# Performance work log

Hardware: AMD Instinct MI355X
Metric: run time of the kernel (lower is better)

The kernel has to match this reference:

```python
import jax, jax.numpy as jnp
import numpy as np

N_NODES = 100000
N_EDGES = 1600000
IN_FEAT = 128
OUT_FEAT = 128


def setup_inputs() -> dict:
    key = jax.random.key(0)
    k1, k2, k3 = jax.random.split(key, 3)
    x = jax.random.normal(k1, (N_NODES, IN_FEAT), dtype=jnp.float32)
    W = jax.random.normal(k2, (IN_FEAT, OUT_FEAT), dtype=jnp.float32) * (1.0 / np.sqrt(IN_FEAT))
    b = jnp.zeros((OUT_FEAT,), dtype=jnp.float32)
    edge_index = jax.random.randint(k3, (2, N_EDGES), 0, N_NODES, dtype=jnp.int64)
    return {"x": x, "W": W, "b": b, "edge_index": edge_index}


def reference(x, W, b, edge_index):
    # PyG GCNConv: add self-loops, symmetric deg normalization, scatter-add.
    N = x.shape[0]
    loops = jnp.arange(N, dtype=edge_index.dtype)
    ei = jnp.concatenate([edge_index, jnp.stack([loops, loops])], axis=1)  # [2, E+N]
    row, col = ei[0], ei[1]  # source, target
    ones = jnp.ones(ei.shape[1], dtype=x.dtype)
    deg = jax.ops.segment_sum(ones, col, num_segments=N)  # in-degree incl. self-loop
    deg_inv_sqrt = jnp.where(deg > 0, jax.lax.rsqrt(deg), 0.0)
    norm = deg_inv_sqrt[row] * deg_inv_sqrt[col]  # [E+N]
    xw = x @ W  # [N, out_feat]
    msg = xw[row] * norm[:, None]  # gather + normalize
    out = jax.ops.segment_sum(msg, col, num_segments=N) + b  # scatter-add + bias
    return out
```

## Files before the change

kernel.cpp:

```cpp
#include <hip/hip_runtime.h>

#define N_NODES 100000
#define N_EDGES 1600000
#define FEAT 128
#define NBUCK 782
#define BUCK_SHIFT 7
#define BUCK_MASK 127
#define GEMM_BLOCKS 1563
#define HIST_EPB 4096
#define HIST_BLOCKS 391
#define WT_PITCH 136

typedef __attribute__((ext_vector_type(8))) short short8;
typedef __attribute__((ext_vector_type(4))) float f32x4;

__device__ inline unsigned short f2bf(float f) {
    unsigned u = __builtin_bit_cast(unsigned, f);
    unsigned r = (u + 0x7FFFu + ((u >> 16) & 1u)) >> 16;
    return (unsigned short)r;
}
__device__ inline float bf2f(unsigned h) {
    unsigned u = h << 16;
    return __builtin_bit_cast(float, u);
}

__global__ __launch_bounds__(256)
void k_gemm_hist(const float* __restrict__ x, const float* __restrict__ W,
                 unsigned short* __restrict__ yb,
                 const int* __restrict__ col, int* __restrict__ bcnt) {
    int bid = blockIdx.x, tid = threadIdx.x;
    if (bid >= GEMM_BLOCKS) {
        __shared__ int hist[NBUCK];
        for (int i = tid; i < NBUCK; i += 256) hist[i] = 0;
        __syncthreads();
        int e0 = (bid - GEMM_BLOCKS) * HIST_EPB;
        int n = min(HIST_EPB, N_EDGES - e0);
        for (int i = tid * 4; i < n; i += 1024) {
            if (i + 3 < n) {
                int4 c4 = *(const int4*)(col + e0 + i);
                atomicAdd(&hist[c4.x >> BUCK_SHIFT], 1);
                atomicAdd(&hist[c4.y >> BUCK_SHIFT], 1);
                atomicAdd(&hist[c4.z >> BUCK_SHIFT], 1);
                atomicAdd(&hist[c4.w >> BUCK_SHIFT], 1);
            } else {
                for (int j = i; j < n; ++j) atomicAdd(&hist[col[e0 + j] >> BUCK_SHIFT], 1);
            }
        }
        __syncthreads();
        for (int i = tid; i < NBUCK; i += 256) {
            int h = hist[i];
            if (h) atomicAdd(&bcnt[i], h);
        }
        return;
    }

    __shared__ unsigned short Ws[FEAT * WT_PITCH];
    for (int idx = tid; idx < FEAT * FEAT; idx += 256) {
        int k = idx >> 7, n = idx & 127;
        Ws[n * WT_PITCH + k] = f2bf(W[idx]);
    }
    __syncthreads();

    int lane = tid & 63;
    int m = lane & 15, quad = lane >> 4;
    int rowBase = bid * 64 + (tid >> 6) * 16;
    int arow = rowBase + m;
    if (arow >= N_NODES) arow = N_NODES - 1;
    const float* xr = x + (size_t)arow * FEAT + quad * 8;

    f32x4 acc[8];
#pragma unroll
    for (int nt = 0; nt < 8; ++nt) acc[nt] = (f32x4){0.f, 0.f, 0.f, 0.f};

#pragma unroll
    for (int kk = 0; kk < 4; ++kk) {
        float4 xa = *(const float4*)(xr + kk * 32);
        float4 xc = *(const float4*)(xr + kk * 32 + 4);
        short8 a;
        a[0] = (short)f2bf(xa.x); a[1] = (short)f2bf(xa.y);
        a[2] = (short)f2bf(xa.z); a[3] = (short)f2bf(xa.w);
        a[4] = (short)f2bf(xc.x); a[5] = (short)f2bf(xc.y);
        a[6] = (short)f2bf(xc.z); a[7] = (short)f2bf(xc.w);
        const unsigned short* wp = Ws + m * WT_PITCH + kk * 32 + quad * 8;
#pragma unroll
        for (int nt = 0; nt < 8; ++nt) {
            short8 bf = *(const short8*)(wp + nt * 16 * WT_PITCH);
            acc[nt] = __builtin_amdgcn_mfma_f32_16x16x32_bf16(a, bf, acc[nt], 0, 0, 0);
        }
    }

    int r0 = rowBase + quad * 4;
#pragma unroll
    for (int nt = 0; nt < 8; ++nt) {
        int cc = nt * 16 + m;
#pragma unroll
        for (int r = 0; r < 4; ++r) {
            int rr = r0 + r;
            if (rr < N_NODES) yb[(size_t)rr * FEAT + cc] = f2bf(acc[nt][r]);
        }
    }
}

__global__ __launch_bounds__(1024)
void k_bscan(const int* __restrict__ bcnt, int* __restrict__ bstarts,
             int* __restrict__ bcursor) {
    __shared__ int s[1024];
    int tid = threadIdx.x;
    int v = (tid < NBUCK) ? bcnt[tid] : 0;
    s[tid] = v;
    __syncthreads();
    for (int off = 1; off < 1024; off <<= 1) {
        int t = (tid >= off) ? s[tid - off] : 0;
        __syncthreads();
        s[tid] += t;
        __syncthreads();
    }
    if (tid < NBUCK) {
        int ex = s[tid] - v;
        bstarts[tid] = ex;
        bcursor[tid] = ex;
    }
    if (tid == NBUCK - 1) bstarts[NBUCK] = s[tid];
}

__global__ __launch_bounds__(256)
void k_bscatter(const int* __restrict__ row, const int* __restrict__ col,
                int* __restrict__ bcursor, unsigned* __restrict__ ebuf) {
    __shared__ int hist[NBUCK];
    __shared__ int gbase[NBUCK];
    int tid = threadIdx.x;
    for (int i = tid; i < NBUCK; i += 256) hist[i] = 0;
    __syncthreads();
    int e0 = blockIdx.x * HIST_EPB;
    int n = min(HIST_EPB, N_EDGES - e0);
    for (int i = tid * 4; i < n; i += 1024) {
        if (i + 3 < n) {
            int4 c4 = *(const int4*)(col + e0 + i);
            atomicAdd(&hist[c4.x >> BUCK_SHIFT], 1);
            atomicAdd(&hist[c4.y >> BUCK_SHIFT], 1);
            atomicAdd(&hist[c4.z >> BUCK_SHIFT], 1);
            atomicAdd(&hist[c4.w >> BUCK_SHIFT], 1);
        } else {
            for (int j = i; j < n; ++j) atomicAdd(&hist[col[e0 + j] >> BUCK_SHIFT], 1);
        }
    }
    __syncthreads();
    for (int i = tid; i < NBUCK; i += 256) {
        int h = hist[i];
        gbase[i] = h ? atomicAdd(&bcursor[i], h) : 0;
    }
    __syncthreads();
    for (int i = tid; i < NBUCK; i += 256) hist[i] = 0;
    __syncthreads();
    for (int i = tid * 4; i < n; i += 1024) {
        if (i + 3 < n) {
            int4 c4 = *(const int4*)(col + e0 + i);
            int4 r4 = *(const int4*)(row + e0 + i);
            int bk, off;
            bk = c4.x >> BUCK_SHIFT; off = atomicAdd(&hist[bk], 1);
            ebuf[gbase[bk] + off] = ((unsigned)r4.x << BUCK_SHIFT) | (unsigned)(c4.x & BUCK_MASK);
            bk = c4.y >> BUCK_SHIFT; off = atomicAdd(&hist[bk], 1);
            ebuf[gbase[bk] + off] = ((unsigned)r4.y << BUCK_SHIFT) | (unsigned)(c4.y & BUCK_MASK);
            bk = c4.z >> BUCK_SHIFT; off = atomicAdd(&hist[bk], 1);
            ebuf[gbase[bk] + off] = ((unsigned)r4.z << BUCK_SHIFT) | (unsigned)(c4.z & BUCK_MASK);
            bk = c4.w >> BUCK_SHIFT; off = atomicAdd(&hist[bk], 1);
            ebuf[gbase[bk] + off] = ((unsigned)r4.w << BUCK_SHIFT) | (unsigned)(c4.w & BUCK_MASK);
        } else {
            for (int j = i; j < n; ++j) {
                int c = col[e0 + j], r = row[e0 + j];
                int bk = c >> BUCK_SHIFT;
                int off = atomicAdd(&hist[bk], 1);
                ebuf[gbase[bk] + off] = ((unsigned)r << BUCK_SHIFT) | (unsigned)(c & BUCK_MASK);
            }
        }
    }
}

__global__ __launch_bounds__(256)
void k_csr(const unsigned* __restrict__ ebuf, const int* __restrict__ bstarts,
           int* __restrict__ starts, float* __restrict__ dinv,
           int* __restrict__ src_idx) {
    __shared__ int hist[128];
    __shared__ int scan[128];
    __shared__ int cur[128];
    int b = blockIdx.x, tid = threadIdx.x;
    int node0 = b << BUCK_SHIFT;
    int nnodes = min(128, N_NODES - node0);
    if (tid < 128) hist[tid] = 0;
    __syncthreads();
    int e0 = bstarts[b], e1 = bstarts[b + 1];
    int ne = e1 - e0;
    for (int i = tid; i < ne; i += 256) atomicAdd(&hist[ebuf[e0 + i] & BUCK_MASK], 1);
    __syncthreads();
    if (tid < 128) scan[tid] = hist[tid];
    __syncthreads();
    for (int off = 1; off < 128; off <<= 1) {
        int t = 0;
        if (tid < 128 && tid >= off) t = scan[tid - off];
        __syncthreads();
        if (tid < 128) scan[tid] += t;
        __syncthreads();
    }
    if (tid < 128) {
        int ex = scan[tid] - hist[tid];
        cur[tid] = ex;
        if (tid < nnodes) {
            starts[node0 + tid] = e0 + ex;
            dinv[node0 + tid] = rsqrtf((float)(hist[tid] + 1));
        }
    }
    if (b == 0 && tid == 0) starts[N_NODES] = N_EDGES;
    __syncthreads();
    for (int i = tid; i < ne; i += 256) {
        unsigned e = ebuf[e0 + i];
        int pos = atomicAdd(&cur[e & BUCK_MASK], 1);
        src_idx[e0 + pos] = (int)(e >> BUCK_SHIFT);
    }
}

#define GATHER_GROUP(D)                                             \
    {                                                               \
        unsigned v[D];                                              \
        _Pragma("unroll")                                           \
        for (int t = 0; t < (D); ++t) {                             \
            int s = __shfl(src, j + t);                             \
            v[t] = y1[(size_t)(unsigned)s * 64 + lane];             \
        }                                                           \
        _Pragma("unroll")                                           \
        for (int t = 0; t < (D); ++t) {                             \
            float d = __shfl(dvv, j + t);                           \
            a0 += d * bf2f(v[t] & 0xFFFFu);                         \
            a1 += d * bf2f(v[t] >> 16);                             \
        }                                                           \
        j += (D);                                                   \
    }

__global__ __launch_bounds__(256)
void k_agg(const unsigned short* __restrict__ yb, const int* __restrict__ starts,
           const int* __restrict__ src_idx, const float* __restrict__ dinv,
           const float* __restrict__ bias, float* __restrict__ out) {
    int node = blockIdx.x * 4 + (threadIdx.x >> 6);
    int lane = threadIdx.x & 63;
    if (node >= N_NODES) return;
    int st = starts[node], en = starts[node + 1];
    float di = dinv[node];
    const unsigned* y1 = (const unsigned*)yb;
    unsigned sv = y1[(size_t)node * 64 + lane];
    float a0 = di * bf2f(sv & 0xFFFFu);
    float a1 = di * bf2f(sv >> 16);
    for (int base = st; base < en; base += 64) {
        int nn = min(64, en - base);
        int src = 0;
        float dvv = 0.f;
        if (lane < nn) {
            src = src_idx[base + lane];
            dvv = dinv[src];
        }
        int j = 0;
        while (j + 16 <= nn) GATHER_GROUP(16)
        if (j + 8 <= nn) GATHER_GROUP(8)
        if (j + 4 <= nn) GATHER_GROUP(4)
        for (; j < nn; ++j) {
            int s = __shfl(src, j);
            float d = __shfl(dvv, j);
            unsigned v = y1[(size_t)(unsigned)s * 64 + lane];
            a0 += d * bf2f(v & 0xFFFFu);
            a1 += d * bf2f(v >> 16);
        }
    }
    float2 bb = ((const float2*)bias)[lane];
    float2 o;
    o.x = bb.x + di * a0;
    o.y = bb.y + di * a1;
    ((float2*)out)[(size_t)node * 64 + lane] = o;
}

extern "C" void kernel_launch(void* const* d_in, const int* in_sizes, int n_in,
                              void* d_out, int out_size, void* d_ws, size_t ws_size,
                              hipStream_t stream) {
    const float* x = (const float*)d_in[0];
    const float* W = (const float*)d_in[1];
    const float* b = (const float*)d_in[2];
    const int* ei = (const int*)d_in[3];
    const int* row = ei;
    const int* col = ei + N_EDGES;
    float* out = (float*)d_out;

    char* ws = (char*)d_ws;
    size_t off = 0;
    auto alloc = [&](size_t bytes) -> void* {
        void* p = ws + off;
        off += (bytes + 511) & ~(size_t)511;
        return p;
    };
    int* bcnt          = (int*)alloc((NBUCK + 1) * 4);
    int* bstarts       = (int*)alloc((NBUCK + 1) * 4);
    int* bcursor       = (int*)alloc((NBUCK + 1) * 4);
    int* starts        = (int*)alloc((size_t)(N_NODES + 1) * 4);
    float* dinv        = (float*)alloc((size_t)N_NODES * 4);
    unsigned* ebuf     = (unsigned*)alloc((size_t)N_EDGES * 4);
    int* src_idx       = (int*)alloc((size_t)N_EDGES * 4);
    unsigned short* yb = (unsigned short*)alloc((size_t)N_NODES * FEAT * 2);

    hipMemsetAsync(bcnt, 0, (NBUCK + 1) * 4, stream);

    k_gemm_hist<<<GEMM_BLOCKS + HIST_BLOCKS, 256, 0, stream>>>(x, W, yb, col, bcnt);
    k_bscan<<<1, 1024, 0, stream>>>(bcnt, bstarts, bcursor);
    k_bscatter<<<HIST_BLOCKS, 256, 0, stream>>>(row, col, bcursor, ebuf);
    k_csr<<<NBUCK, 256, 0, stream>>>(ebuf, bstarts, starts, dinv, src_idx);
    k_agg<<<(N_NODES + 3) / 4, 256, 0, stream>>>(yb, starts, src_idx, dinv, b, out);
}
```

Before: 233.6 us.

## Fuse CSR build into bucket aggregation, compute degrees via global atomics

Removes the separate k_csr kernel by building each bucket's per-node edge lists in shared memory inside k_agg. Each 512-thread block now handles one 128-node bucket, and the per-source degree comes from a global deg array filled with atomics in the histogram phase. The GEMM is also restructured so each block computes 128 rows, swapping operand roles so bf16 results can be stored as packed uint2 writes. The goal is to cut a kernel launch and the src_idx/starts/dinv round trips through memory. The cost is 1.6M global atomics on deg and fewer, larger aggregation blocks, which may lower occupancy and load balance, plus a slow fallback path for buckets with more than 4096 edges.

```diff
diff --git a/kernel.cpp b/kernel.cpp
--- a/kernel.cpp
+++ b/kernel.cpp
@@ -6,10 +6,12 @@
 #define NBUCK 782
 #define BUCK_SHIFT 7
 #define BUCK_MASK 127
-#define GEMM_BLOCKS 1563
+#define GEMM_ROWS 128
+#define GEMM_BLOCKS 782
 #define HIST_EPB 4096
 #define HIST_BLOCKS 391
 #define WT_PITCH 136
+#define AGG_CAP 4096
 
 typedef __attribute__((ext_vector_type(8))) short short8;
 typedef __attribute__((ext_vector_type(4))) float f32x4;
@@ -25,9 +27,10 @@
 }
 
 __global__ __launch_bounds__(256)
-void k_gemm_hist(const float* __restrict__ x, const float* __restrict__ W,
-                 unsigned short* __restrict__ yb,
-                 const int* __restrict__ col, int* __restrict__ bcnt) {
+void k_gemm_deg(const float* __restrict__ x, const float* __restrict__ W,
+                unsigned short* __restrict__ yb,
+                const int* __restrict__ col, int* __restrict__ bcnt,
+                int* __restrict__ deg) {
     int bid = blockIdx.x, tid = threadIdx.x;
     if (bid >= GEMM_BLOCKS) {
         __shared__ int hist[NBUCK];
@@ -42,8 +45,16 @@
                 atomicAdd(&hist[c4.y >> BUCK_SHIFT], 1);
                 atomicAdd(&hist[c4.z >> BUCK_SHIFT], 1);
                 atomicAdd(&hist[c4.w >> BUCK_SHIFT], 1);
+                atomicAdd(&deg[c4.x], 1);
+                atomicAdd(&deg[c4.y], 1);
+                atomicAdd(&deg[c4.z], 1);
+                atomicAdd(&deg[c4.w], 1);
             } else {
-                for (int j = i; j < n; ++j) atomicAdd(&hist[col[e0 + j] >> BUCK_SHIFT], 1);
+                for (int j = i; j < n; ++j) {
+                    int c = col[e0 + j];
+                    atomicAdd(&hist[c >> BUCK_SHIFT], 1);
+                    atomicAdd(&deg[c], 1);
+                }
             }
         }
         __syncthreads();
@@ -56,47 +67,72 @@
 
     __shared__ unsigned short Ws[FEAT * WT_PITCH];
     for (int idx = tid; idx < FEAT * FEAT; idx += 256) {
-        int k = idx >> 7, n = idx & 127;
-        Ws[n * WT_PITCH + k] = f2bf(W[idx]);
+        int k = idx >> 7, f = idx & 127;
+        Ws[f * WT_PITCH + k] = f2bf(W[idx]);
     }
     __syncthreads();
 
     int lane = tid & 63;
     int m = lane & 15, quad = lane >> 4;
-    int rowBase = bid * 64 + (tid >> 6) * 16;
-    int arow = rowBase + m;
-    if (arow >= N_NODES) arow = N_NODES - 1;
-    const float* xr = x + (size_t)arow * FEAT + quad * 8;
-
-    f32x4 acc[8];
-#pragma unroll
-    for (int nt = 0; nt < 8; ++nt) acc[nt] = (f32x4){0.f, 0.f, 0.f, 0.f};
+    int w = tid >> 6;
+    int nodeA = bid * GEMM_ROWS + w * 16 + m;
+    int nodeB = nodeA + 64;
+    int ldA = nodeA < N_NODES ? nodeA : N_NODES - 1;
+    int ldB = nodeB < N_NODES ? nodeB : N_NODES - 1;
+    const float* xA = x + (size_t)ldA * FEAT + quad * 8;
+    const float* xB = x + (size_t)ldB * FEAT + quad * 8;
+
+    f32x4 accA[8], accB[8];
+#pragma unroll
+    for (int nt = 0; nt < 8; ++nt) {
+        accA[nt] = (f32x4){0.f, 0.f, 0.f, 0.f};
+        accB[nt] = (f32x4){0.f, 0.f, 0.f, 0.f};
+    }
 
 #pragma unroll
     for (int kk = 0; kk < 4; ++kk) {
-        float4 xa = *(const float4*)(xr + kk * 32);
-        float4 xc = *(const float4*)(xr + kk * 32 + 4);
-        short8 a;
-        a[0] = (short)f2bf(xa.x); a[1] = (short)f2bf(xa.y);
-        a[2] = (short)f2bf(xa.z); a[3] = (short)f2bf(xa.w);
-        a[4] = (short)f2bf(xc.x); a[5] = (short)f2bf(xc.y);
-        a[6] = (short)f2bf(xc.z); a[7] = (short)f2bf(xc.w);
-        const unsigned short* wp = Ws + m * WT_PITCH + kk * 32 + quad * 8;
+        float4 a0v = *(const float4*)(xA + kk * 32);
+        float4 a1v = *(const float4*)(xA + kk * 32 + 4);
+        float4 b0v = *(const float4*)(xB + kk * 32);
+        float4 b1v = *(const float4*)(xB + kk * 32 + 4);
+        short8 fa, fb;
+        fa[0] = (short)f2bf(a0v.x); fa[1] = (short)f2bf(a0v.y);
+        fa[2] = (short)f2bf(a0v.z); fa[3] = (short)f2bf(a0v.w);
+        fa[4] = (short)f2bf(a1v.x); fa[5] = (short)f2bf(a1v.y);
+        fa[6] = (short)f2bf(a1v.z); fa[7] = (short)f2bf(a1v.w);
+        fb[0] = (short)f2bf(b0v.x); fb[1] = (short)f2bf(b0v.y);
+        fb[2] = (short)f2bf(b0v.z); fb[3] = (short)f2bf(b0v.w);
+        fb[4] = (short)f2bf(b1v.x); fb[5] = (short)f2bf(b1v.y);
+        fb[6] = (short)f2bf(b1v.z); fb[7] = (short)f2bf(b1v.w);
+        const unsigned short* wp = Ws + kk * 32 + quad * 8;
 #pragma unroll
         for (int nt = 0; nt < 8; ++nt) {
-            short8 bf = *(const short8*)(wp + nt * 16 * WT_PITCH);
-            acc[nt] = __builtin_amdgcn_mfma_f32_16x16x32_bf16(a, bf, acc[nt], 0, 0, 0);
-        }
-    }
-
-    int r0 = rowBase + quad * 4;
-#pragma unroll
-    for (int nt = 0; nt < 8; ++nt) {
-        int cc = nt * 16 + m;
-#pragma unroll
-        for (int r = 0; r < 4; ++r) {
-            int rr = r0 + r;
-            if (rr < N_NODES) yb[(size_t)rr * FEAT + cc] = f2bf(acc[nt][r]);
+            short8 af = *(const short8*)(wp + (nt * 16 + m) * WT_PITCH);
+            accA[nt] = __builtin_amdgcn_mfma_f32_16x16x32_bf16(af, fa, accA[nt], 0, 0, 0);
+            accB[nt] = __builtin_amdgcn_mfma_f32_16x16x32_bf16(af, fb, accB[nt], 0, 0, 0);
+        }
+    }
+
+    if (nodeA < N_NODES) {
+        unsigned* yp = (unsigned*)(yb + (size_t)nodeA * FEAT);
+#pragma unroll
+        for (int nt = 0; nt < 8; ++nt) {
+            int u0 = nt * 8 + quad * 2;
+            uint2 pk;
+            pk.x = (unsigned)f2bf(accA[nt][0]) | ((unsigned)f2bf(accA[nt][1]) << 16);
+            pk.y = (unsigned)f2bf(accA[nt][2]) | ((unsigned)f2bf(accA[nt][3]) << 16);
+            *(uint2*)(yp + u0) = pk;
+        }
+    }
+    if (nodeB < N_NODES) {
+        unsigned* yp = (unsigned*)(yb + (size_t)nodeB * FEAT);
+#pragma unroll
+        for (int nt = 0; nt < 8; ++nt) {
+            int u0 = nt * 8 + quad * 2;
+            uint2 pk;
+            pk.x = (unsigned)f2bf(accB[nt][0]) | ((unsigned)f2bf(accB[nt][1]) << 16);
+            pk.y = (unsigned)f2bf(accB[nt][2]) | ((unsigned)f2bf(accB[nt][3]) << 16);
+            *(uint2*)(yp + u0) = pk;
         }
     }
 }
@@ -176,48 +212,6 @@
     }
 }
 
-__global__ __launch_bounds__(256)
-void k_csr(const unsigned* __restrict__ ebuf, const int* __restrict__ bstarts,
-           int* __restrict__ starts, float* __restrict__ dinv,
-           int* __restrict__ src_idx) {
-    __shared__ int hist[128];
-    __shared__ int scan[128];
-    __shared__ int cur[128];
-    int b = blockIdx.x, tid = threadIdx.x;
-    int node0 = b << BUCK_SHIFT;
-    int nnodes = min(128, N_NODES - node0);
-    if (tid < 128) hist[tid] = 0;
-    __syncthreads();
-    int e0 = bstarts[b], e1 = bstarts[b + 1];
-    int ne = e1 - e0;
-    for (int i = tid; i < ne; i += 256) atomicAdd(&hist[ebuf[e0 + i] & BUCK_MASK], 1);
-    __syncthreads();
-    if (tid < 128) scan[tid] = hist[tid];
-    __syncthreads();
-    for (int off = 1; off < 128; off <<= 1) {
-        int t = 0;
-        if (tid < 128 && tid >= off) t = scan[tid - off];
-        __syncthreads();
-        if (tid < 128) scan[tid] += t;
-        __syncthreads();
-    }
-    if (tid < 128) {
-        int ex = scan[tid] - hist[tid];
-        cur[tid] = ex;
-        if (tid < nnodes) {
-            starts[node0 + tid] = e0 + ex;
-            dinv[node0 + tid] = rsqrtf((float)(hist[tid] + 1));
-        }
-    }
-    if (b == 0 && tid == 0) starts[N_NODES] = N_EDGES;
-    __syncthreads();
-    for (int i = tid; i < ne; i += 256) {
-        unsigned e = ebuf[e0 + i];
-        int pos = atomicAdd(&cur[e & BUCK_MASK], 1);
-        src_idx[e0 + pos] = (int)(e >> BUCK_SHIFT);
-    }
-}
-
 #define GATHER_GROUP(D)                                             \
     {                                                               \
         unsigned v[D];                                              \
@@ -235,44 +229,104 @@
         j += (D);                                                   \
     }
 
-__global__ __launch_bounds__(256)
-void k_agg(const unsigned short* __restrict__ yb, const int* __restrict__ starts,
-           const int* __restrict__ src_idx, const float* __restrict__ dinv,
+__global__ __launch_bounds__(512)
+void k_agg(const unsigned short* __restrict__ yb, const unsigned* __restrict__ ebuf,
+           const int* __restrict__ bstarts, const int* __restrict__ deg,
            const float* __restrict__ bias, float* __restrict__ out) {
-    int node = blockIdx.x * 4 + (threadIdx.x >> 6);
-    int lane = threadIdx.x & 63;
-    if (node >= N_NODES) return;
-    int st = starts[node], en = starts[node + 1];
-    float di = dinv[node];
+    __shared__ int hist[128];
+    __shared__ int stl[128];
+    __shared__ int cur[128];
+    __shared__ int srcs[AGG_CAP];
+    int b = blockIdx.x, tid = threadIdx.x;
+    int node0 = b << BUCK_SHIFT;
+    int e0 = bstarts[b], e1 = bstarts[b + 1];
+    int ne = e1 - e0;
+    if (tid < 128) hist[tid] = 0;
+    __syncthreads();
+    for (int i = tid; i < ne; i += 512) atomicAdd(&hist[ebuf[e0 + i] & BUCK_MASK], 1);
+    __syncthreads();
+
+    int wv = tid >> 6, lane = tid & 63;
     const unsigned* y1 = (const unsigned*)yb;
-    unsigned sv = y1[(size_t)node * 64 + lane];
-    float a0 = di * bf2f(sv & 0xFFFFu);
-    float a1 = di * bf2f(sv >> 16);
-    for (int base = st; base < en; base += 64) {
-        int nn = min(64, en - base);
-        int src = 0;
-        float dvv = 0.f;
-        if (lane < nn) {
-            src = src_idx[base + lane];
-            dvv = dinv[src];
-        }
-        int j = 0;
-        while (j + 16 <= nn) GATHER_GROUP(16)
-        if (j + 8 <= nn) GATHER_GROUP(8)
-        if (j + 4 <= nn) GATHER_GROUP(4)
-        for (; j < nn; ++j) {
-            int s = __shfl(src, j);
-            float d = __shfl(dvv, j);
-            unsigned v = y1[(size_t)(unsigned)s * 64 + lane];
-            a0 += d * bf2f(v & 0xFFFFu);
-            a1 += d * bf2f(v >> 16);
-        }
-    }
     float2 bb = ((const float2*)bias)[lane];
-    float2 o;
-    o.x = bb.x + di * a0;
-    o.y = bb.y + di * a1;
-    ((float2*)out)[(size_t)node * 64 + lane] = o;
+
+    if (ne > AGG_CAP) {
+        for (int it = 0; it < 16; ++it) {
+            int t = wv * 16 + it, node = node0 + t;
+            if (node >= N_NODES) break;
+            float di = rsqrtf((float)(hist[t] + 1));
+            unsigned sv = y1[(size_t)node * 64 + lane];
+            float a0 = di * bf2f(sv & 0xFFFFu), a1 = di * bf2f(sv >> 16);
+            for (int e = e0; e < e1; ++e) {
+                unsigned ev = ebuf[e];
+                if ((int)(ev & BUCK_MASK) == t) {
+                    int s = (int)(ev >> BUCK_SHIFT);
+                    float dv = rsqrtf((float)(deg[s] + 1));
+                    unsigned v = y1[(size_t)(unsigned)s * 64 + lane];
+                    a0 += dv * bf2f(v & 0xFFFFu);
+                    a1 += dv * bf2f(v >> 16);
+                }
+            }
+            float2 o;
+            o.x = bb.x + di * a0;
+            o.y = bb.y + di * a1;
+            ((float2*)out)[(size_t)node * 64 + lane] = o;
+        }
+        return;
+    }
+
+    if (tid < 128) stl[tid] = hist[tid];
+    __syncthreads();
+    for (int off = 1; off < 128; off <<= 1) {
+        int t = 0;
+        if (tid < 128 && tid >= off) t = stl[tid - off];
+        __syncthreads();
+        if (tid < 128) stl[tid] += t;
+        __syncthreads();
+    }
+    if (tid < 128) cur[tid] = stl[tid] - hist[tid];
+    __syncthreads();
+    for (int i = tid; i < ne; i += 512) {
+        unsigned e = ebuf[e0 + i];
+        int pos = atomicAdd(&cur[e & BUCK_MASK], 1);
+        srcs[pos] = (int)(e >> BUCK_SHIFT);
+    }
+    __syncthreads();
+
+    for (int it = 0; it < 16; ++it) {
+        int t = wv * 16 + it;
+        int node = node0 + t;
+        if (node >= N_NODES) break;
+        int st = stl[t] - hist[t], en = stl[t];
+        float di = rsqrtf((float)(hist[t] + 1));
+        unsigned sv = y1[(size_t)node * 64 + lane];
+        float a0 = di * bf2f(sv & 0xFFFFu);
+        float a1 = di * bf2f(sv >> 16);
+        for (int base = st; base < en; base += 64) {
+            int nn = min(64, en - base);
+            int src = 0;
+            float dvv = 0.f;
+            if (lane < nn) {
+                src = srcs[base + lane];
+                dvv = rsqrtf((float)(deg[src] + 1));
+            }
+            int j = 0;
+            while (j + 16 <= nn) GATHER_GROUP(16)
+            if (j + 8 <= nn) GATHER_GROUP(8)
+            if (j + 4 <= nn) GATHER_GROUP(4)
+            for (; j < nn; ++j) {
+                int s = __shfl(src, j);
+                float d = __shfl(dvv, j);
+                unsigned v = y1[(size_t)(unsigned)s * 64 + lane];
+                a0 += d * bf2f(v & 0xFFFFu);
+                a1 += d * bf2f(v >> 16);
+            }
+        }
+        float2 o;
+        o.x = bb.x + di * a0;
+        o.y = bb.y + di * a1;
+        ((float2*)out)[(size_t)node * 64 + lane] = o;
+    }
 }
 
 extern "C" void kernel_launch(void* const* d_in, const int* in_sizes, int n_in,
@@ -294,19 +348,17 @@
         return p;
     };
     int* bcnt          = (int*)alloc((NBUCK + 1) * 4);
+    int* deg           = (int*)alloc((size_t)N_NODES * 4);
     int* bstarts       = (int*)alloc((NBUCK + 1) * 4);
     int* bcursor       = (int*)alloc((NBUCK + 1) * 4);
-    int* starts        = (int*)alloc((size_t)(N_NODES + 1) * 4);
-    float* dinv        = (float*)alloc((size_t)N_NODES * 4);
     unsigned* ebuf     = (unsigned*)alloc((size_t)N_EDGES * 4);
-    int* src_idx       = (int*)alloc((size_t)N_EDGES * 4);
     unsigned short* yb = (unsigned short*)alloc((size_t)N_NODES * FEAT * 2);
 
-    hipMemsetAsync(bcnt, 0, (NBUCK + 1) * 4, stream);
-
-    k_gemm_hist<<<GEMM_BLOCKS + HIST_BLOCKS, 256, 0, stream>>>(x, W, yb, col, bcnt);
+    size_t msz = (size_t)((char*)deg - (char*)bcnt) + (size_t)N_NODES * 4;
+    hipMemsetAsync(bcnt, 0, msz, stream);
+
+    k_gemm_deg<<<GEMM_BLOCKS + HIST_BLOCKS, 256, 0, stream>>>(x, W, yb, col, bcnt, deg);
     k_bscan<<<1, 1024, 0, stream>>>(bcnt, bstarts, bcursor);
     k_bscatter<<<HIST_BLOCKS, 256, 0, stream>>>(row, col, bcursor, ebuf);
-    k_csr<<<NBUCK, 256, 0, stream>>>(ebuf, bstarts, starts, dinv, src_idx);
-    k_agg<<<(N_NODES + 3) / 4, 256, 0, stream>>>(yb, starts, src_idx, dinv, b, out);
-}
+    k_agg<<<NBUCK, 512, 0, stream>>>(yb, ebuf, bstarts, deg, b, out);
+}
```

After: 310.3 us. 32.8% more time.

## Fuse bucket scan into scatter kernel and transpose GEMM MFMA for packed stores

Applied to the files above, without the earlier changes.

Removes the separate single-block bucket-scan launch: every scatter block now recomputes the 782-bucket prefix sum redundantly from bcnt and adds its own atomic cursor offset, and block 0 writes bstarts. The scatter kernel now uses 125 blocks of 12800 edges instead of 391 blocks of 4096. The GEMM swaps its MFMA operands so each lane holds one node's outputs, which allows packed 8-byte bf16 stores instead of scattered 2-byte stores. The trade is some redundant scan work in each block, fewer blocks in the scatter phase, and one fewer kernel launch.

```diff
diff --git a/kernel.cpp b/kernel.cpp
--- a/kernel.cpp
+++ b/kernel.cpp
@@ -9,6 +9,8 @@
 #define GEMM_BLOCKS 1563
 #define HIST_EPB 4096
 #define HIST_BLOCKS 391
+#define SCAT_EPB 12800
+#define SCAT_BLOCKS 125
 #define WT_PITCH 136
 
 typedef __attribute__((ext_vector_type(8))) short short8;
@@ -56,17 +58,16 @@
 
     __shared__ unsigned short Ws[FEAT * WT_PITCH];
     for (int idx = tid; idx < FEAT * FEAT; idx += 256) {
-        int k = idx >> 7, n = idx & 127;
-        Ws[n * WT_PITCH + k] = f2bf(W[idx]);
+        int k = idx >> 7, f = idx & 127;
+        Ws[f * WT_PITCH + k] = f2bf(W[idx]);
     }
     __syncthreads();
 
     int lane = tid & 63;
     int m = lane & 15, quad = lane >> 4;
-    int rowBase = bid * 64 + (tid >> 6) * 16;
-    int arow = rowBase + m;
-    if (arow >= N_NODES) arow = N_NODES - 1;
-    const float* xr = x + (size_t)arow * FEAT + quad * 8;
+    int node = bid * 64 + (tid >> 6) * 16 + m;
+    int ldn = node < N_NODES ? node : N_NODES - 1;
+    const float* xr = x + (size_t)ldn * FEAT + quad * 8;
 
     f32x4 acc[8];
 #pragma unroll
@@ -76,63 +77,68 @@
     for (int kk = 0; kk < 4; ++kk) {
         float4 xa = *(const float4*)(xr + kk * 32);
         float4 xc = *(const float4*)(xr + kk * 32 + 4);
-        short8 a;
-        a[0] = (short)f2bf(xa.x); a[1] = (short)f2bf(xa.y);
-        a[2] = (short)f2bf(xa.z); a[3] = (short)f2bf(xa.w);
-        a[4] = (short)f2bf(xc.x); a[5] = (short)f2bf(xc.y);
-        a[6] = (short)f2bf(xc.z); a[7] = (short)f2bf(xc.w);
-        const unsigned short* wp = Ws + m * WT_PITCH + kk * 32 + quad * 8;
+        short8 fx;
+        fx[0] = (short)f2bf(xa.x); fx[1] = (short)f2bf(xa.y);
+        fx[2] = (short)f2bf(xa.z); fx[3] = (short)f2bf(xa.w);
+        fx[4] = (short)f2bf(xc.x); fx[5] = (short)f2bf(xc.y);
+        fx[6] = (short)f2bf(xc.z); fx[7] = (short)f2bf(xc.w);
+        const unsigned short* wp = Ws + kk * 32 + quad * 8;
 #pragma unroll
         for (int nt = 0; nt < 8; ++nt) {
-            short8 bf = *(const short8*)(wp + nt * 16 * WT_PITCH);
-            acc[nt] = __builtin_amdgcn_mfma_f32_16x16x32_bf16(a, bf, acc[nt], 0, 0, 0);
-        }
-    }
-
-    int r0 = rowBase + quad * 4;
+            short8 af = *(const short8*)(wp + (nt * 16 + m) * WT_PITCH);
+            acc[nt] = __builtin_amdgcn_mfma_f32_16x16x32_bf16(af, fx, acc[nt], 0, 0, 0);
+        }
+    }
+
+    if (node < N_NODES) {
+        unsigned* yp = (unsigned*)(yb + (size_t)node * FEAT);
 #pragma unroll
-    for (int nt = 0; nt < 8; ++nt) {
-        int cc = nt * 16 + m;
-#pragma unroll
-        for (int r = 0; r < 4; ++r) {
-            int rr = r0 + r;
-            if (rr < N_NODES) yb[(size_t)rr * FEAT + cc] = f2bf(acc[nt][r]);
-        }
-    }
-}
-
-__global__ __launch_bounds__(1024)
-void k_bscan(const int* __restrict__ bcnt, int* __restrict__ bstarts,
-             int* __restrict__ bcursor) {
-    __shared__ int s[1024];
-    int tid = threadIdx.x;
-    int v = (tid < NBUCK) ? bcnt[tid] : 0;
-    s[tid] = v;
-    __syncthreads();
-    for (int off = 1; off < 1024; off <<= 1) {
-        int t = (tid >= off) ? s[tid - off] : 0;
-        __syncthreads();
-        s[tid] += t;
-        __syncthreads();
-    }
-    if (tid < NBUCK) {
-        int ex = s[tid] - v;
-        bstarts[tid] = ex;
-        bcursor[tid] = ex;
-    }
-    if (tid == NBUCK - 1) bstarts[NBUCK] = s[tid];
+        for (int nt = 0; nt < 8; ++nt) {
+            uint2 pk;
+            pk.x = (unsigned)f2bf(acc[nt][0]) | ((unsigned)f2bf(acc[nt][1]) << 16);
+            pk.y = (unsigned)f2bf(acc[nt][2]) | ((unsigned)f2bf(acc[nt][3]) << 16);
+            *(uint2*)(yp + nt * 8 + quad * 2) = pk;
+        }
+    }
 }
 
 __global__ __launch_bounds__(256)
 void k_bscatter(const int* __restrict__ row, const int* __restrict__ col,
-                int* __restrict__ bcursor, unsigned* __restrict__ ebuf) {
+                const int* __restrict__ bcnt, int* __restrict__ bcur0,
+                int* __restrict__ bstarts, unsigned* __restrict__ ebuf) {
+    __shared__ int sb[1024];
+    __shared__ int csum[256];
+    __shared__ int bstartsL[NBUCK];
     __shared__ int hist[NBUCK];
     __shared__ int gbase[NBUCK];
     int tid = threadIdx.x;
+
+    for (int i = tid; i < 1024; i += 256) sb[i] = (i < NBUCK) ? bcnt[i] : 0;
+    __syncthreads();
+    int v0 = sb[tid * 4], v1 = sb[tid * 4 + 1], v2 = sb[tid * 4 + 2], v3 = sb[tid * 4 + 3];
+    int p1 = v0 + v1, p2 = p1 + v2, p3 = p2 + v3;
+    csum[tid] = p3;
+    __syncthreads();
+    for (int off = 1; off < 256; off <<= 1) {
+        int t = (tid >= off) ? csum[tid - off] : 0;
+        __syncthreads();
+        csum[tid] += t;
+        __syncthreads();
+    }
+    int base = csum[tid] - p3;
+    if (tid * 4 < NBUCK)     bstartsL[tid * 4]     = base;
+    if (tid * 4 + 1 < NBUCK) bstartsL[tid * 4 + 1] = base + v0;
+    if (tid * 4 + 2 < NBUCK) bstartsL[tid * 4 + 2] = base + p1;
+    if (tid * 4 + 3 < NBUCK) bstartsL[tid * 4 + 3] = base + p2;
     for (int i = tid; i < NBUCK; i += 256) hist[i] = 0;
     __syncthreads();
-    int e0 = blockIdx.x * HIST_EPB;
-    int n = min(HIST_EPB, N_EDGES - e0);
+    if (blockIdx.x == 0) {
+        for (int i = tid; i < NBUCK; i += 256) bstarts[i] = bstartsL[i];
+        if (tid == 0) bstarts[NBUCK] = N_EDGES;
+    }
+
+    int e0 = blockIdx.x * SCAT_EPB;
+    int n = min(SCAT_EPB, N_EDGES - e0);
     for (int i = tid * 4; i < n; i += 1024) {
         if (i + 3 < n) {
             int4 c4 = *(const int4*)(col + e0 + i);
@@ -147,7 +153,7 @@
     __syncthreads();
     for (int i = tid; i < NBUCK; i += 256) {
         int h = hist[i];
-        gbase[i] = h ? atomicAdd(&bcursor[i], h) : 0;
+        gbase[i] = bstartsL[i] + (h ? atomicAdd(&bcur0[i], h) : 0);
     }
     __syncthreads();
     for (int i = tid; i < NBUCK; i += 256) hist[i] = 0;
@@ -294,19 +300,19 @@
         return p;
     };
     int* bcnt          = (int*)alloc((NBUCK + 1) * 4);
+    int* bcur0         = (int*)alloc((NBUCK + 1) * 4);
     int* bstarts       = (int*)alloc((NBUCK + 1) * 4);
-    int* bcursor       = (int*)alloc((NBUCK + 1) * 4);
     int* starts        = (int*)alloc((size_t)(N_NODES + 1) * 4);
     float* dinv        = (float*)alloc((size_t)N_NODES * 4);
     unsigned* ebuf     = (unsigned*)alloc((size_t)N_EDGES * 4);
     int* src_idx       = (int*)alloc((size_t)N_EDGES * 4);
     unsigned short* yb = (unsigned short*)alloc((size_t)N_NODES * FEAT * 2);
 
-    hipMemsetAsync(bcnt, 0, (NBUCK + 1) * 4, stream);
+    size_t msz = (size_t)((char*)bcur0 - (char*)bcnt) + (size_t)(NBUCK + 1) * 4;
+    hipMemsetAsync(bcnt, 0, msz, stream);
 
     k_gemm_hist<<<GEMM_BLOCKS + HIST_BLOCKS, 256, 0, stream>>>(x, W, yb, col, bcnt);
-    k_bscan<<<1, 1024, 0, stream>>>(bcnt, bstarts, bcursor);
-    k_bscatter<<<HIST_BLOCKS, 256, 0, stream>>>(row, col, bcursor, ebuf);
+    k_bscatter<<<SCAT_BLOCKS, 256, 0, stream>>>(row, col, bcnt, bcur0, bstarts, ebuf);
     k_csr<<<NBUCK, 256, 0, stream>>>(ebuf, bstarts, starts, dinv, src_idx);
     k_agg<<<(N_NODES + 3) / 4, 256, 0, stream>>>(yb, starts, src_idx, dinv, b, out);
 }
```

Result: no change. 236.6 us (+1.3%).
